# Optimization experiments

Measured on AMD Instinct MI355X. Metric: run time of the kernel, lower is better.

Reference implementation:

```python
import jax, jax.numpy as jnp
import numpy as np

B, C, H, W = 16, 512, 32, 32
CQ = C // 8  # 64
EPS = 1e-5


def _conv1x1(x, Wt, b=None):
    # x: (B,C,H,W), Wt: (O,C) -> (B,O,H,W)
    y = jnp.einsum('bchw,oc->bohw', x, Wt)
    if b is not None:
        y = y + b[None, :, None, None]
    return y


def setup_inputs() -> dict:
    key = jax.random.key(0)
    ks = jax.random.split(key, 12)
    s = 0.02
    return {
        'rgb':    jax.random.normal(ks[0], (B, C, H, W), jnp.float32),
        'depth':  jax.random.normal(ks[1], (B, C, H, W), jnp.float32),
        'Wq_rgb': jax.random.normal(ks[2], (CQ, C), jnp.float32) * s,
        'bq_rgb': jnp.zeros((CQ,), jnp.float32),
        'Wk_dep': jax.random.normal(ks[3], (CQ, C), jnp.float32) * s,
        'bk_dep': jnp.zeros((CQ,), jnp.float32),
        'Wv_dep': jax.random.normal(ks[4], (C, C), jnp.float32) * s,
        'bv_dep': jnp.zeros((C,), jnp.float32),
        'Wq_dep': jax.random.normal(ks[5], (CQ, C), jnp.float32) * s,
        'bq_dep': jnp.zeros((CQ,), jnp.float32),
        'Wk_rgb': jax.random.normal(ks[6], (CQ, C), jnp.float32) * s,
        'bk_rgb': jnp.zeros((CQ,), jnp.float32),
        'Wv_rgb': jax.random.normal(ks[7], (C, C), jnp.float32) * s,
        'bv_rgb': jnp.zeros((C,), jnp.float32),
        'W_fuse': jax.random.normal(ks[8], (C, 2 * C), jnp.float32) * s,
        'gamma':  jnp.ones((C,), jnp.float32),
        'beta':   jnp.zeros((C,), jnp.float32),
    }


def reference(rgb, depth, Wq_rgb, bq_rgb, Wk_dep, bk_dep, Wv_dep, bv_dep,
              Wq_dep, bq_dep, Wk_rgb, bk_rgb, Wv_rgb, bv_rgb, W_fuse, gamma, beta):
    b, c, h, w = rgb.shape
    hw = h * w
    scale = jnp.asarray(c, rgb.dtype) ** 0.5  # note: full C, as in source

    # RGB attends to depth
    q = _conv1x1(rgb, Wq_rgb, bq_rgb).reshape(b, -1, hw).transpose(0, 2, 1)   # (B,HW,CQ)
    k = _conv1x1(depth, Wk_dep, bk_dep).reshape(b, -1, hw)                    # (B,CQ,HW)
    v = _conv1x1(depth, Wv_dep, bv_dep).reshape(b, -1, hw).transpose(0, 2, 1) # (B,HW,C)
    attn = jax.nn.softmax(jnp.einsum('bnd,bdm->bnm', q, k) / scale, axis=-1)
    rgb_att = jnp.einsum('bnm,bmc->bnc', attn, v).transpose(0, 2, 1).reshape(b, c, h, w)

    # Depth attends to RGB
    q2 = _conv1x1(depth, Wq_dep, bq_dep).reshape(b, -1, hw).transpose(0, 2, 1)
    k2 = _conv1x1(rgb, Wk_rgb, bk_rgb).reshape(b, -1, hw)
    v2 = _conv1x1(rgb, Wv_rgb, bv_rgb).reshape(b, -1, hw).transpose(0, 2, 1)
    attn2 = jax.nn.softmax(jnp.einsum('bnd,bdm->bnm', q2, k2) / scale, axis=-1)
    dep_att = jnp.einsum('bnm,bmc->bnc', attn2, v2).transpose(0, 2, 1).reshape(b, c, h, w)

    cat = jnp.concatenate([rgb_att, dep_att], axis=1)      # (B,2C,H,W)
    fused = jnp.einsum('bchw,oc->bohw', cat, W_fuse)        # 1x1 conv, no bias

    # BatchNorm2d in training mode (batch statistics, biased variance)
    mean = fused.mean(axis=(0, 2, 3))
    var = fused.var(axis=(0, 2, 3))
    normed = (fused - mean[None, :, None, None]) * jax.lax.rsqrt(var + EPS)[None, :, None, None]
    out = normed * gamma[None, :, None, None] + beta[None, :, None, None]
    return jax.nn.relu(out)
```

## Files before the change

kernel.cpp:

```cpp
#include <hip/hip_runtime.h>
#include <math.h>

#define NB 16
#define CC 512
#define CQ 64
#define HWN 1024

typedef float4 f4;
typedef __bf16 bf16x8 __attribute__((ext_vector_type(8)));
typedef float f32x4 __attribute__((ext_vector_type(4)));
typedef __attribute__((ext_vector_type(8))) unsigned short ushort8v;

__device__ __forceinline__ unsigned short f2bf(float f) {
    unsigned int u = __float_as_uint(f);
    u = (u + 0x7fffu + ((u >> 16) & 1u)) >> 16;
    return (unsigned short)u;
}
__device__ __forceinline__ float bf2f(unsigned short u) {
    return __uint_as_float(((unsigned int)u) << 16);
}

__device__ __forceinline__ void gload16(const unsigned short* g, unsigned short* l) {
    __builtin_amdgcn_global_load_lds(
        (const __attribute__((address_space(1))) unsigned int*)g,
        (__attribute__((address_space(3))) unsigned int*)l,
        16, 0, 0);
}

template<int BM, int BN, int BIAS, bool OBF16, int ZSH, bool STATS>
__global__ __launch_bounds__(256)
void mfma_g(const unsigned short* __restrict__ A, long sAlo, long sAhi, int lda,
            const unsigned short* __restrict__ B, long sBlo, long sBhi, int ldb,
            const float* __restrict__ bias, long sBiasHi,
            void* __restrict__ Cout, long sClo, long sChi, int ldc,
            int Ksize, float alpha, float* __restrict__ statsAcc)
{
    constexpr int MF = BM / 32;
    constexpr int NF = BN / 32;
    constexpr int CA = BM / 32;
    constexpr int CB = BN / 32;
    __shared__ unsigned short As[2][BM * 64];
    __shared__ unsigned short Bs[2][BN * 64];

    const int gx = gridDim.x, gy = gridDim.y;
    int f = blockIdx.x + gx * (blockIdx.y + gy * blockIdx.z);
    const int nwg = gx * gy * gridDim.z;
    f = (f & 7) * (nwg >> 3) + (f >> 3);
    const int bx = f % gx; const int t2 = f / gx;
    const int by = t2 % gy; const int bz = t2 / gy;

    const int zlo = ZSH ? (bz & ((1 << ZSH) - 1)) : 0;
    const int zhi = bz >> ZSH;

    const int t = threadIdx.x, lane = t & 63, wid = t >> 6;
    const int wm = (wid >> 1) * (BM / 2), wn = (wid & 1) * (BN / 2);
    const int m0 = by * BM, n0 = bx * BN;
    const unsigned short* Ab = A + (long)zlo * sAlo + (long)zhi * sAhi;
    const unsigned short* Bb = B + (long)zlo * sBlo + (long)zhi * sBhi;

    const int srow = lane >> 3;
    const int scol = ((lane & 7) ^ srow) << 3;
    const unsigned short* gA[CA]; const unsigned short* gB[CB];
    unsigned short* lA[CA]; unsigned short* lB[CB];
#pragma unroll
    for (int c = 0; c < CA; ++c) {
        const int seg = wid + 4 * c;
        gA[c] = Ab + (long)(m0 + seg * 8 + srow) * lda + scol;
        lA[c] = &As[0][seg * 512];
    }
#pragma unroll
    for (int c = 0; c < CB; ++c) {
        const int seg = wid + 4 * c;
        gB[c] = Bb + (long)(n0 + seg * 8 + srow) * ldb + scol;
        lB[c] = &Bs[0][seg * 512];
    }

    f32x4 acc[MF][NF] = {};
    const int l15 = lane & 15, slot = lane >> 4;

#pragma unroll
    for (int c = 0; c < CA; ++c) gload16(gA[c], lA[c]);
#pragma unroll
    for (int c = 0; c < CB; ++c) gload16(gB[c], lB[c]);
    __syncthreads();

    const int nt = Ksize >> 6;
    int cur = 0;
    for (int tt = 0; tt < nt; ++tt) {
        if (tt + 1 < nt) {
            const int ko = (tt + 1) << 6;
            const int nb = cur ^ 1;
#pragma unroll
            for (int c = 0; c < CA; ++c) gload16(gA[c] + ko, lA[c] + nb * (BM * 64));
#pragma unroll
            for (int c = 0; c < CB; ++c) gload16(gB[c] + ko, lB[c] + nb * (BN * 64));
        }
        bf16x8 alo[MF], ahi[MF], blo[NF], bhi[NF];
#pragma unroll
        for (int i = 0; i < MF; ++i) {
            const int r = wm + i * 16 + l15;
            alo[i] = *(const bf16x8*)&As[cur][r * 64 + ((slot ^ (r & 7)) << 3)];
            ahi[i] = *(const bf16x8*)&As[cur][r * 64 + (((slot + 4) ^ (r & 7)) << 3)];
        }
#pragma unroll
        for (int j = 0; j < NF; ++j) {
            const int r = wn + j * 16 + l15;
            blo[j] = *(const bf16x8*)&Bs[cur][r * 64 + ((slot ^ (r & 7)) << 3)];
            bhi[j] = *(const bf16x8*)&Bs[cur][r * 64 + (((slot + 4) ^ (r & 7)) << 3)];
        }
#pragma unroll
        for (int i = 0; i < MF; ++i)
#pragma unroll
            for (int j = 0; j < NF; ++j) {
                acc[i][j] = __builtin_amdgcn_mfma_f32_16x16x32_bf16(alo[i], blo[j], acc[i][j], 0, 0, 0);
                acc[i][j] = __builtin_amdgcn_mfma_f32_16x16x32_bf16(ahi[i], bhi[j], acc[i][j], 0, 0, 0);
            }
        __syncthreads();
        cur ^= 1;
    }

    unsigned short* C16 = (unsigned short*)Cout + (long)zlo * sClo + (long)zhi * sChi;
    float*          C32 = (float*)Cout + (long)zlo * sClo + (long)zhi * sChi;
    const float* biasb = (BIAS != 0) ? bias + (long)zhi * sBiasHi : nullptr;
    const int r0 = slot << 2;
#pragma unroll
    for (int i = 0; i < MF; ++i) {
#pragma unroll
        for (int r = 0; r < 4; ++r) {
            const int m = m0 + wm + i * 16 + r0 + r;
            const float brow = (BIAS == 1) ? biasb[m] : 0.0f;
            float ps = 0.0f, ps2 = 0.0f;
#pragma unroll
            for (int j = 0; j < NF; ++j) {
                const int n = n0 + wn + j * 16 + l15;
                const float bb = (BIAS == 2) ? biasb[n] : brow;
                const float o = alpha * (acc[i][j][r] + bb);
                if (OBF16) C16[(long)m * ldc + n] = f2bf(o);
                else       C32[(long)m * ldc + n] = o;
                if (STATS) { ps += o; ps2 += o * o; }
            }
            if (STATS) {
#pragma unroll
                for (int off = 8; off; off >>= 1) {
                    ps  += __shfl_xor(ps, off);
                    ps2 += __shfl_xor(ps2, off);
                }
                if (l15 == 0) {
                    const int slot2 = ((zlo * gx + bx) << 1) + (wid & 1);
                    statsAcc[(long)m * 256 + slot2]          = ps;
                    statsAcc[131072 + (long)m * 256 + slot2] = ps2;
                }
            }
        }
    }
}

__global__ __launch_bounds__(256)
void attn_fused2(const unsigned short* __restrict__ QK, unsigned short* __restrict__ Pcat)
{
    __shared__ unsigned short Es[16 * 1024];
    const int t = threadIdx.x, lane = t & 63, w = t >> 6;
    int p = blockIdx.x + 64 * (blockIdx.y + 16 * blockIdx.z);
    p = (p & 7) * 256 + (p >> 3);
    const int bx = p & 63, b = (p >> 6) & 15, dir = p >> 10;
    const unsigned short* Q = QK + (long)(dir ? b : 16 + b) * 131072;
    const unsigned short* K = QK + (long)(dir ? 16 + b : b) * 131072 + 64;
    const int l15 = lane & 15, slot = lane >> 4, kg = slot << 3;

    const long mrow = (long)bx * 16 + l15;
    bf16x8 aq0 = *(const bf16x8*)&Q[mrow * 128 + kg];
    bf16x8 aq1 = *(const bf16x8*)&Q[mrow * 128 + 32 + kg];

    const int colbase = w << 8;
    const int rbase = slot << 2;
#pragma unroll
    for (int c = 0; c < 4; ++c) {
        const int n0 = colbase + (c << 6);
        bf16x8 bk0[4], bk1[4];
#pragma unroll
        for (int j = 0; j < 4; ++j) {
            const long krow = n0 + (j << 4) + l15;
            bk0[j] = *(const bf16x8*)&K[krow * 128 + kg];
            bk1[j] = *(const bf16x8*)&K[krow * 128 + 32 + kg];
        }
#pragma unroll
        for (int j = 0; j < 4; ++j) {
            f32x4 a = {0.f, 0.f, 0.f, 0.f};
            a = __builtin_amdgcn_mfma_f32_16x16x32_bf16(aq0, bk0[j], a, 0, 0, 0);
            a = __builtin_amdgcn_mfma_f32_16x16x32_bf16(aq1, bk1[j], a, 0, 0, 0);
            const int col = n0 + (j << 4) + l15;
#pragma unroll
            for (int r = 0; r < 4; ++r) {
                const int row = rbase + r;
                Es[(row << 10) + (col ^ (row << 3))] = f2bf(__expf(a[r]));
            }
        }
    }
    __syncthreads();

#pragma unroll
    for (int rr = 0; rr < 4; ++rr) {
        const int R = (w << 2) + rr;
        const int base = R << 10, sw = R << 3;
        const int c8 = lane << 3;
        ushort8v u0 = *(const ushort8v*)&Es[base + (c8 ^ sw)];
        ushort8v u1 = *(const ushort8v*)&Es[base + ((c8 + 512) ^ sw)];
        float v[16];
#pragma unroll
        for (int i = 0; i < 8; ++i) { v[i] = bf2f(u0[i]); v[8 + i] = bf2f(u1[i]); }
        float s = 0.0f;
#pragma unroll
        for (int i = 0; i < 16; ++i) s += v[i];
#pragma unroll
        for (int off = 32; off; off >>= 1) s += __shfl_xor(s, off);
        const float inv = 1.0f / s;
        ushort8v o0, o1;
#pragma unroll
        for (int i = 0; i < 8; ++i) { o0[i] = f2bf(v[i] * inv); o1[i] = f2bf(v[8 + i] * inv); }
        unsigned short* dst = Pcat + ((long)(b * 1024 + bx * 16 + R)) * 2048
                            + dir * 1024 + c8;
        *(ushort8v*)dst = o0;
        *(ushort8v*)(dst + 512) = o1;
    }
}

__global__ __launch_bounds__(256)
void transpose_cvt2(const float* __restrict__ src_dep, const float* __restrict__ src_rgb,
                    unsigned short* __restrict__ dst)
{
    __shared__ float tile[64][65];
    const int t = threadIdx.x;
    const int z = blockIdx.z;
    const float* s = (z < 16 ? src_dep : src_rgb) + (long)(z & 15) * 524288;
    unsigned short* d = dst + (long)z * 524288;
    const int c0 = blockIdx.x << 6, r0 = blockIdx.y << 6;
    const int lr = t >> 4, lc = (t & 15) << 2;
#pragma unroll
    for (int i = 0; i < 4; ++i) {
        f4 v = *(const f4*)(s + (long)(r0 + lr + i * 16) * HWN + c0 + lc);
        *(f4*)&tile[lr + i * 16][lc] = v;
    }
    __syncthreads();
#pragma unroll
    for (int i = 0; i < 4; ++i) {
        const int crow = lr + i * 16;
        ushort4 o;
        o.x = f2bf(tile[lc + 0][crow]);
        o.y = f2bf(tile[lc + 1][crow]);
        o.z = f2bf(tile[lc + 2][crow]);
        o.w = f2bf(tile[lc + 3][crow]);
        *(ushort4*)&d[(long)(c0 + crow) * CC + r0 + lc] = o;
    }
}

__global__ __launch_bounds__(256)
void transpose_cvtW(const float* __restrict__ w0, const float* __restrict__ w1,
                    unsigned short* __restrict__ dst)
{
    __shared__ float tile[64][65];
    const int t = threadIdx.x;
    const int z = blockIdx.z;
    const float* src = z ? w1 : w0;
    unsigned short* d = dst + (long)z * 262144;
    const int c0 = blockIdx.x << 6, r0 = blockIdx.y << 6;
    const int lr = t >> 4, lc = (t & 15) << 2;
#pragma unroll
    for (int i = 0; i < 4; ++i) {
        f4 v = *(const f4*)(src + (long)(r0 + lr + i * 16) * CC + c0 + lc);
        *(f4*)&tile[lr + i * 16][lc] = v;
    }
    __syncthreads();
#pragma unroll
    for (int i = 0; i < 4; ++i) {
        const int crow = lr + i * 16;
        ushort4 o;
        o.x = f2bf(tile[lc + 0][crow]);
        o.y = f2bf(tile[lc + 1][crow]);
        o.z = f2bf(tile[lc + 2][crow]);
        o.w = f2bf(tile[lc + 3][crow]);
        *(ushort4*)&d[(long)(c0 + crow) * CC + r0 + lc] = o;
    }
}

__global__ __launch_bounds__(256)
void cvt_flat(const float* __restrict__ src, unsigned short* __restrict__ dst, int n4)
{
    const int i = blockIdx.x * 256 + threadIdx.x;
    if (i < n4) {
        f4 v = ((const f4*)src)[i];
        ushort4 o;
        o.x = f2bf(v.x); o.y = f2bf(v.y); o.z = f2bf(v.z); o.w = f2bf(v.w);
        ((ushort4*)dst)[i] = o;
    }
}

__global__ __launch_bounds__(256)
void prep_wqk(const float* __restrict__ wqd, const float* __restrict__ wkd,
              const float* __restrict__ wqr, const float* __restrict__ wkr,
              unsigned short* __restrict__ dst, float s)
{
    const int i4 = blockIdx.x * 256 + threadIdx.x;
    const int row = i4 >> 7;
    const int seg = row >> 6;
    const float* src = (seg == 0) ? wqd : (seg == 1) ? wkd : (seg == 2) ? wqr : wkr;
    const float sc = (seg & 1) ? 1.0f : s;
    f4 v = ((const f4*)src)[((row & 63) << 7) + (i4 & 127)];
    ushort4 o;
    o.x = f2bf(v.x * sc); o.y = f2bf(v.y * sc); o.z = f2bf(v.z * sc); o.w = f2bf(v.w * sc);
    ((ushort4*)dst)[i4] = o;
}

__global__ __launch_bounds__(256)
void prep_bias(const float* __restrict__ bqd, const float* __restrict__ bkd,
               const float* __restrict__ bqr, const float* __restrict__ bkr,
               float* __restrict__ dst, float s)
{
    const int t = threadIdx.x;
    float v;
    if (t < 64)       v = bqd[t] * s;
    else if (t < 128) v = bkd[t - 64];
    else if (t < 192) v = bqr[t - 128] * s;
    else              v = bkr[t - 192];
    dst[t] = v;
}

__global__ __launch_bounds__(256)
void bfuse_k(const float* __restrict__ Wf, const float* __restrict__ bv1,
             const float* __restrict__ bv2, float* __restrict__ bfuse)
{
    const int o = blockIdx.x, t = threadIdx.x;
    const float* row = Wf + (long)o * 1024;
    float s = row[t] * bv1[t] + row[512 + t] * bv2[t]
            + row[256 + t] * bv1[256 + t] + row[768 + t] * bv2[256 + t];
#pragma unroll
    for (int off = 32; off; off >>= 1) s += __shfl_xor(s, off);
    __shared__ float r[4];
    if ((t & 63) == 0) r[t >> 6] = s;
    __syncthreads();
    if (t == 0) bfuse[o] = r[0] + r[1] + r[2] + r[3];
}

__global__ __launch_bounds__(256)
void bn_finalize(const float* __restrict__ part, float* __restrict__ stats)
{
    const int c = blockIdx.x, t = threadIdx.x;
    float s1 = part[(long)c * 256 + t];
    float s2 = part[131072 + (long)c * 256 + t];
#pragma unroll
    for (int off = 32; off; off >>= 1) {
        s1 += __shfl_xor(s1, off);
        s2 += __shfl_xor(s2, off);
    }
    __shared__ float r1[4], r2[4];
    if ((t & 63) == 0) { r1[t >> 6] = s1; r2[t >> 6] = s2; }
    __syncthreads();
    if (t == 0) {
        const float S1 = r1[0] + r1[1] + r1[2] + r1[3];
        const float S2 = r2[0] + r2[1] + r2[2] + r2[3];
        const float mean = S1 * (1.0f / 16384.0f);
        const float var  = S2 * (1.0f / 16384.0f) - mean * mean;
        stats[c]      = mean;
        stats[CC + c] = rsqrtf(var + 1e-5f);
    }
}

__global__ __launch_bounds__(256)
void bn_apply_bf16(const unsigned short* __restrict__ fused, const float* __restrict__ stats,
                   const float* __restrict__ gamma, const float* __restrict__ beta,
                   float* __restrict__ out)
{
    const long i8 = (long)blockIdx.x * 256 + threadIdx.x;
    ushort8v v = ((const ushort8v*)fused)[i8];
    const int o = (int)((i8 >> 7) & 511);
    const float is = stats[CC + o];
    const float g  = gamma[o] * is;
    const float bb = beta[o] - stats[o] * g;
    f4 o0, o1;
    o0.x = fmaxf(fmaf(bf2f(v[0]), g, bb), 0.0f);
    o0.y = fmaxf(fmaf(bf2f(v[1]), g, bb), 0.0f);
    o0.z = fmaxf(fmaf(bf2f(v[2]), g, bb), 0.0f);
    o0.w = fmaxf(fmaf(bf2f(v[3]), g, bb), 0.0f);
    o1.x = fmaxf(fmaf(bf2f(v[4]), g, bb), 0.0f);
    o1.y = fmaxf(fmaf(bf2f(v[5]), g, bb), 0.0f);
    o1.z = fmaxf(fmaf(bf2f(v[6]), g, bb), 0.0f);
    o1.w = fmaxf(fmaf(bf2f(v[7]), g, bb), 0.0f);
    ((f4*)out)[i8 * 2]     = o0;
    ((f4*)out)[i8 * 2 + 1] = o1;
}

static constexpr long B_depT  = 0;
static constexpr long B_rgbT  = 16777216;
static constexpr long B_WvT1  = 33554432;
static constexpr long B_Wfb   = 34603008;
static constexpr long B_Wqk   = 35651584;
static constexpr long B_Wc1   = 35913728;
static constexpr long B_bfu   = 36962304;
static constexpr long B_bias  = 36964352;
static constexpr long B_QK    = 36966400;
static constexpr long B_Acat  = 45355008;
static constexpr long B_Pcat  = 78909440;
static constexpr long B_fused = 146018304;
static constexpr long B_stats = 179572736;
static constexpr long B_part  = 179576832;

extern "C" void kernel_launch(void* const* d_in, const int* in_sizes, int n_in,
                              void* d_out, int out_size, void* d_ws, size_t ws_size,
                              hipStream_t stream)
{
    const float* rgb    = (const float*)d_in[0];
    const float* depth  = (const float*)d_in[1];
    const float* Wq_rgb = (const float*)d_in[2];
    const float* bq_rgb = (const float*)d_in[3];
    const float* Wk_dep = (const float*)d_in[4];
    const float* bk_dep = (const float*)d_in[5];
    const float* Wv_dep = (const float*)d_in[6];
    const float* bv_dep = (const float*)d_in[7];
    const float* Wq_dep = (const float*)d_in[8];
    const float* bq_dep = (const float*)d_in[9];
    const float* Wk_rgb = (const float*)d_in[10];
    const float* bk_rgb = (const float*)d_in[11];
    const float* Wv_rgb = (const float*)d_in[12];
    const float* bv_rgb = (const float*)d_in[13];
    const float* W_fuse = (const float*)d_in[14];
    const float* gamma  = (const float*)d_in[15];
    const float* beta   = (const float*)d_in[16];
    char* ws = (char*)d_ws;
    float* out = (float*)d_out;

    const float inv_scale = 0.044194173824159223f;
    dim3 blk(256);

    unsigned short* depT = (unsigned short*)(ws + B_depT);
    unsigned short* WvT1 = (unsigned short*)(ws + B_WvT1);
    unsigned short* Wfb  = (unsigned short*)(ws + B_Wfb);
    unsigned short* Wqk  = (unsigned short*)(ws + B_Wqk);
    unsigned short* Wc1  = (unsigned short*)(ws + B_Wc1);
    float*          bfu  = (float*)(ws + B_bfu);
    float*          bias = (float*)(ws + B_bias);
    unsigned short* QK   = (unsigned short*)(ws + B_QK);
    unsigned short* Acat = (unsigned short*)(ws + B_Acat);
    unsigned short* Pcat = (unsigned short*)(ws + B_Pcat);
    unsigned short* fused= (unsigned short*)(ws + B_fused);
    float*          stats= (float*)(ws + B_stats);
    float*          part = (float*)(ws + B_part);

    transpose_cvt2<<<dim3(16, 8, 32), blk, 0, stream>>>(depth, rgb, depT);
    transpose_cvtW<<<dim3(8, 8, 2), blk, 0, stream>>>(Wv_dep, Wv_rgb, WvT1);
    cvt_flat<<<512, blk, 0, stream>>>(W_fuse, Wfb, 131072);
    prep_wqk<<<128, blk, 0, stream>>>(Wq_dep, Wk_dep, Wq_rgb, Wk_rgb, Wqk, inv_scale);
    prep_bias<<<1, blk, 0, stream>>>(bq_dep, bk_dep, bq_rgb, bk_rgb, bias, inv_scale);
    bfuse_k<<<512, blk, 0, stream>>>(W_fuse, bv_dep, bv_rgb, bfu);

    mfma_g<128, 128, 0, true, 0, false><<<dim3(4, 4, 2), blk, 0, stream>>>(
        Wfb, 0, 512, 1024, WvT1, 0, 262144, 512, nullptr, 0,
        Wc1, 0, 262144, 512, 512, 1.0f, nullptr);

    mfma_g<128, 128, 2, true, 4, false><<<dim3(1, 8, 32), blk, 0, stream>>>(
        depT, 524288, 8388608, 512, Wqk, 0, 65536, 512, bias, 128,
        QK, 131072, 2097152, 128, 512, 1.0f, nullptr);

    mfma_g<128, 128, 0, true, 4, false><<<dim3(8, 4, 32), blk, 0, stream>>>(
        Wc1, 0, 262144, 512, depT, 524288, 8388608, 512, nullptr, 0,
        Acat, 1048576, 1024, 2048, 512, 1.0f, nullptr);

    attn_fused2<<<dim3(64, NB, 2), blk, 0, stream>>>(QK, Pcat);

    mfma_g<128, 128, 1, true, 4, true><<<dim3(8, 4, 16), blk, 0, stream>>>(
        Acat, 1048576, 0, 2048, Pcat, 2097152, 0, 2048, bfu, 0,
        fused, 524288, 0, 1024, 2048, 1.0f, part);

    bn_finalize<<<512, blk, 0, stream>>>(part, stats);
    bn_apply_bf16<<<4096, blk, 0, stream>>>(fused, stats, gamma, beta, out);
}
```

Before: 175.3 us.

## Keep softmax exponentials in registers and merge weight-prep kernels into one launch

New measurement: 171.1 us. -2.4%, faster.

```diff
diff --git a/kernel.cpp b/kernel.cpp
--- a/kernel.cpp
+++ b/kernel.cpp
@@ -156,13 +156,11 @@
 }
 
 __global__ __launch_bounds__(256)
-void attn_fused2(const unsigned short* __restrict__ QK, unsigned short* __restrict__ Pcat)
-{
-    __shared__ unsigned short Es[16 * 1024];
+void attn_fused3(const unsigned short* __restrict__ QK, unsigned short* __restrict__ Pcat)
+{
+    __shared__ float ws16[16][4];
     const int t = threadIdx.x, lane = t & 63, w = t >> 6;
-    int p = blockIdx.x + 64 * (blockIdx.y + 16 * blockIdx.z);
-    p = (p & 7) * 256 + (p >> 3);
-    const int bx = p & 63, b = (p >> 6) & 15, dir = p >> 10;
+    const int bx = blockIdx.x, b = blockIdx.y, dir = blockIdx.z;
     const unsigned short* Q = QK + (long)(dir ? b : 16 + b) * 131072;
     const unsigned short* K = QK + (long)(dir ? 16 + b : b) * 131072 + 64;
     const int l15 = lane & 15, slot = lane >> 4, kg = slot << 3;
@@ -173,6 +171,8 @@
 
     const int colbase = w << 8;
     const int rbase = slot << 2;
+    f32x4 e[4][4];
+    float rowp[4] = {0.0f, 0.0f, 0.0f, 0.0f};
 #pragma unroll
     for (int c = 0; c < 4; ++c) {
         const int n0 = colbase + (c << 6);
@@ -188,39 +188,40 @@
             f32x4 a = {0.f, 0.f, 0.f, 0.f};
             a = __builtin_amdgcn_mfma_f32_16x16x32_bf16(aq0, bk0[j], a, 0, 0, 0);
             a = __builtin_amdgcn_mfma_f32_16x16x32_bf16(aq1, bk1[j], a, 0, 0, 0);
-            const int col = n0 + (j << 4) + l15;
 #pragma unroll
             for (int r = 0; r < 4; ++r) {
-                const int row = rbase + r;
-                Es[(row << 10) + (col ^ (row << 3))] = f2bf(__expf(a[r]));
+                const float ev = __expf(a[r]);
+                e[c][j][r] = ev;
+                rowp[r] += ev;
             }
         }
     }
+#pragma unroll
+    for (int off = 1; off < 16; off <<= 1) {
+#pragma unroll
+        for (int r = 0; r < 4; ++r) rowp[r] += __shfl_xor(rowp[r], off);
+    }
+    if (l15 == 0) {
+#pragma unroll
+        for (int r = 0; r < 4; ++r) ws16[rbase + r][w] = rowp[r];
+    }
     __syncthreads();
-
-#pragma unroll
-    for (int rr = 0; rr < 4; ++rr) {
-        const int R = (w << 2) + rr;
-        const int base = R << 10, sw = R << 3;
-        const int c8 = lane << 3;
-        ushort8v u0 = *(const ushort8v*)&Es[base + (c8 ^ sw)];
-        ushort8v u1 = *(const ushort8v*)&Es[base + ((c8 + 512) ^ sw)];
-        float v[16];
-#pragma unroll
-        for (int i = 0; i < 8; ++i) { v[i] = bf2f(u0[i]); v[8 + i] = bf2f(u1[i]); }
-        float s = 0.0f;
-#pragma unroll
-        for (int i = 0; i < 16; ++i) s += v[i];
-#pragma unroll
-        for (int off = 32; off; off >>= 1) s += __shfl_xor(s, off);
-        const float inv = 1.0f / s;
-        ushort8v o0, o1;
-#pragma unroll
-        for (int i = 0; i < 8; ++i) { o0[i] = f2bf(v[i] * inv); o1[i] = f2bf(v[8 + i] * inv); }
-        unsigned short* dst = Pcat + ((long)(b * 1024 + bx * 16 + R)) * 2048
-                            + dir * 1024 + c8;
-        *(ushort8v*)dst = o0;
-        *(ushort8v*)(dst + 512) = o1;
+    float inv[4];
+#pragma unroll
+    for (int r = 0; r < 4; ++r) {
+        f4 s = *(const f4*)ws16[rbase + r];
+        inv[r] = 1.0f / (s.x + s.y + s.z + s.w);
+    }
+    unsigned short* dstb = Pcat + ((long)(b * 1024 + bx * 16)) * 2048 + dir * 1024;
+#pragma unroll
+    for (int c = 0; c < 4; ++c) {
+#pragma unroll
+        for (int j = 0; j < 4; ++j) {
+            const int col = colbase + (c << 6) + (j << 4) + l15;
+#pragma unroll
+            for (int r = 0; r < 4; ++r)
+                dstb[(long)(rbase + r) * 2048 + col] = f2bf(e[c][j][r] * inv[r]);
+        }
     }
 }
 
@@ -254,90 +255,78 @@
 }
 
 __global__ __launch_bounds__(256)
-void transpose_cvtW(const float* __restrict__ w0, const float* __restrict__ w1,
-                    unsigned short* __restrict__ dst)
+void prep_all(const float* __restrict__ Wv_dep, const float* __restrict__ Wv_rgb,
+              const float* __restrict__ W_fuse,
+              const float* __restrict__ wqd, const float* __restrict__ wkd,
+              const float* __restrict__ wqr, const float* __restrict__ wkr,
+              const float* __restrict__ bqd, const float* __restrict__ bkd,
+              const float* __restrict__ bqr, const float* __restrict__ bkr,
+              const float* __restrict__ bvd, const float* __restrict__ bvr,
+              unsigned short* __restrict__ WvT, unsigned short* __restrict__ Wfb,
+              unsigned short* __restrict__ Wqk, float* __restrict__ bfuse,
+              float* __restrict__ biascat, float s)
 {
     __shared__ float tile[64][65];
-    const int t = threadIdx.x;
-    const int z = blockIdx.z;
-    const float* src = z ? w1 : w0;
-    unsigned short* d = dst + (long)z * 262144;
-    const int c0 = blockIdx.x << 6, r0 = blockIdx.y << 6;
-    const int lr = t >> 4, lc = (t & 15) << 2;
-#pragma unroll
-    for (int i = 0; i < 4; ++i) {
-        f4 v = *(const f4*)(src + (long)(r0 + lr + i * 16) * CC + c0 + lc);
-        *(f4*)&tile[lr + i * 16][lc] = v;
-    }
-    __syncthreads();
-#pragma unroll
-    for (int i = 0; i < 4; ++i) {
-        const int crow = lr + i * 16;
-        ushort4 o;
-        o.x = f2bf(tile[lc + 0][crow]);
-        o.y = f2bf(tile[lc + 1][crow]);
-        o.z = f2bf(tile[lc + 2][crow]);
-        o.w = f2bf(tile[lc + 3][crow]);
-        *(ushort4*)&d[(long)(c0 + crow) * CC + r0 + lc] = o;
-    }
-}
-
-__global__ __launch_bounds__(256)
-void cvt_flat(const float* __restrict__ src, unsigned short* __restrict__ dst, int n4)
-{
-    const int i = blockIdx.x * 256 + threadIdx.x;
-    if (i < n4) {
-        f4 v = ((const f4*)src)[i];
+    const int blk = blockIdx.x, t = threadIdx.x;
+
+    if (blk < 128) {
+        const int z = blk >> 6, tx = blk & 63;
+        const float* src = z ? Wv_rgb : Wv_dep;
+        unsigned short* d = WvT + (long)z * 262144;
+        const int c0 = (tx & 7) << 6, r0 = (tx >> 3) << 6;
+        const int lr = t >> 4, lc = (t & 15) << 2;
+#pragma unroll
+        for (int i = 0; i < 4; ++i) {
+            f4 v = *(const f4*)(src + (long)(r0 + lr + i * 16) * CC + c0 + lc);
+            *(f4*)&tile[lr + i * 16][lc] = v;
+        }
+        __syncthreads();
+#pragma unroll
+        for (int i = 0; i < 4; ++i) {
+            const int crow = lr + i * 16;
+            ushort4 o;
+            o.x = f2bf(tile[lc + 0][crow]);
+            o.y = f2bf(tile[lc + 1][crow]);
+            o.z = f2bf(tile[lc + 2][crow]);
+            o.w = f2bf(tile[lc + 3][crow]);
+            *(ushort4*)&d[(long)(c0 + crow) * CC + r0 + lc] = o;
+        }
+    } else if (blk < 640) {
+        const int i4 = (blk - 128) * 256 + t;
+        f4 v = ((const f4*)W_fuse)[i4];
         ushort4 o;
         o.x = f2bf(v.x); o.y = f2bf(v.y); o.z = f2bf(v.z); o.w = f2bf(v.w);
-        ((ushort4*)dst)[i] = o;
-    }
-}
-
-__global__ __launch_bounds__(256)
-void prep_wqk(const float* __restrict__ wqd, const float* __restrict__ wkd,
-              const float* __restrict__ wqr, const float* __restrict__ wkr,
-              unsigned short* __restrict__ dst, float s)
-{
-    const int i4 = blockIdx.x * 256 + threadIdx.x;
-    const int row = i4 >> 7;
-    const int seg = row >> 6;
-    const float* src = (seg == 0) ? wqd : (seg == 1) ? wkd : (seg == 2) ? wqr : wkr;
-    const float sc = (seg & 1) ? 1.0f : s;
-    f4 v = ((const f4*)src)[((row & 63) << 7) + (i4 & 127)];
-    ushort4 o;
-    o.x = f2bf(v.x * sc); o.y = f2bf(v.y * sc); o.z = f2bf(v.z * sc); o.w = f2bf(v.w * sc);
-    ((ushort4*)dst)[i4] = o;
-}
-
-__global__ __launch_bounds__(256)
-void prep_bias(const float* __restrict__ bqd, const float* __restrict__ bkd,
-               const float* __restrict__ bqr, const float* __restrict__ bkr,
-               float* __restrict__ dst, float s)
-{
-    const int t = threadIdx.x;
-    float v;
-    if (t < 64)       v = bqd[t] * s;
-    else if (t < 128) v = bkd[t - 64];
-    else if (t < 192) v = bqr[t - 128] * s;
-    else              v = bkr[t - 192];
-    dst[t] = v;
-}
-
-__global__ __launch_bounds__(256)
-void bfuse_k(const float* __restrict__ Wf, const float* __restrict__ bv1,
-             const float* __restrict__ bv2, float* __restrict__ bfuse)
-{
-    const int o = blockIdx.x, t = threadIdx.x;
-    const float* row = Wf + (long)o * 1024;
-    float s = row[t] * bv1[t] + row[512 + t] * bv2[t]
-            + row[256 + t] * bv1[256 + t] + row[768 + t] * bv2[256 + t];
-#pragma unroll
-    for (int off = 32; off; off >>= 1) s += __shfl_xor(s, off);
-    __shared__ float r[4];
-    if ((t & 63) == 0) r[t >> 6] = s;
-    __syncthreads();
-    if (t == 0) bfuse[o] = r[0] + r[1] + r[2] + r[3];
+        ((ushort4*)Wfb)[i4] = o;
+    } else if (blk < 768) {
+        const int i4 = (blk - 640) * 256 + t;
+        const int row = i4 >> 7;
+        const int seg = row >> 6;
+        const float* src = (seg == 0) ? wqd : (seg == 1) ? wkd : (seg == 2) ? wqr : wkr;
+        const float sc = (seg & 1) ? 1.0f : s;
+        f4 v = ((const f4*)src)[((row & 63) << 7) + (i4 & 127)];
+        ushort4 o;
+        o.x = f2bf(v.x * sc); o.y = f2bf(v.y * sc);
+        o.z = f2bf(v.z * sc); o.w = f2bf(v.w * sc);
+        ((ushort4*)Wqk)[i4] = o;
+    } else if (blk < 1280) {
+        const int o = blk - 768;
+        const float* row = W_fuse + (long)o * 1024;
+        float sum = row[t] * bvd[t] + row[512 + t] * bvr[t]
+                  + row[256 + t] * bvd[256 + t] + row[768 + t] * bvr[256 + t];
+#pragma unroll
+        for (int off = 32; off; off >>= 1) sum += __shfl_xor(sum, off);
+        float* red = &tile[0][0];
+        if ((t & 63) == 0) red[t >> 6] = sum;
+        __syncthreads();
+        if (t == 0) bfuse[o] = red[0] + red[1] + red[2] + red[3];
+    } else {
+        float v;
+        if (t < 64)       v = bqd[t] * s;
+        else if (t < 128) v = bkd[t - 64];
+        else if (t < 192) v = bqr[t - 128] * s;
+        else              v = bkr[t - 192];
+        biascat[t] = v;
+    }
 }
 
 __global__ __launch_bounds__(256)
@@ -445,11 +434,9 @@
     float*          part = (float*)(ws + B_part);
 
     transpose_cvt2<<<dim3(16, 8, 32), blk, 0, stream>>>(depth, rgb, depT);
-    transpose_cvtW<<<dim3(8, 8, 2), blk, 0, stream>>>(Wv_dep, Wv_rgb, WvT1);
-    cvt_flat<<<512, blk, 0, stream>>>(W_fuse, Wfb, 131072);
-    prep_wqk<<<128, blk, 0, stream>>>(Wq_dep, Wk_dep, Wq_rgb, Wk_rgb, Wqk, inv_scale);
-    prep_bias<<<1, blk, 0, stream>>>(bq_dep, bk_dep, bq_rgb, bk_rgb, bias, inv_scale);
-    bfuse_k<<<512, blk, 0, stream>>>(W_fuse, bv_dep, bv_rgb, bfu);
+    prep_all<<<1281, blk, 0, stream>>>(Wv_dep, Wv_rgb, W_fuse,
+        Wq_dep, Wk_dep, Wq_rgb, Wk_rgb, bq_dep, bk_dep, bq_rgb, bk_rgb,
+        bv_dep, bv_rgb, WvT1, Wfb, Wqk, bfu, bias, inv_scale);
 
     mfma_g<128, 128, 0, true, 0, false><<<dim3(4, 4, 2), blk, 0, stream>>>(
         Wfb, 0, 512, 1024, WvT1, 0, 262144, 512, nullptr, 0,
@@ -463,7 +450,7 @@
         Wc1, 0, 262144, 512, depT, 524288, 8388608, 512, nullptr, 0,
         Acat, 1048576, 1024, 2048, 512, 1.0f, nullptr);
 
-    attn_fused2<<<dim3(64, NB, 2), blk, 0, stream>>>(QK, Pcat);
+    attn_fused3<<<dim3(64, NB, 2), blk, 0, stream>>>(QK, Pcat);
 
     mfma_g<128, 128, 1, true, 4, true><<<dim3(8, 4, 16), blk, 0, stream>>>(
         Acat, 1048576, 0, 2048, Pcat, 2097152, 0, 2048, bfu, 0,
```
